# Kernel optimization log

Measured on AMD Instinct MI355X. Metric: run time of the kernel, lower is better.

The kernel has to match this reference:

```python
import jax, jax.numpy as jnp
import numpy as np

N_NODES = 100000
N_EDGES = 800000
F_IN = 128
H1, C1 = 8, 32
N_CLS = 40
NEG_SLOPE = 0.2


def setup_inputs() -> dict:
    key = jax.random.key(0)
    ks = jax.random.split(key, 10)
    s = 1.0 / np.sqrt(F_IN)
    s2 = 1.0 / np.sqrt(H1 * C1)
    return {
        "x": jax.random.normal(ks[0], (N_NODES, F_IN), jnp.float32),
        "edge_index": jax.random.randint(ks[1], (2, N_EDGES), 0, N_NODES, jnp.int64),
        "W1": jax.random.normal(ks[2], (F_IN, H1 * C1), jnp.float32) * s,
        "a_src1": jax.random.normal(ks[3], (H1, C1), jnp.float32) * s2,
        "a_dst1": jax.random.normal(ks[4], (H1, C1), jnp.float32) * s2,
        "b1": jnp.zeros((H1 * C1,), jnp.float32),
        "W2": jax.random.normal(ks[5], (H1 * C1, N_CLS), jnp.float32) * s2,
        "a_src2": jax.random.normal(ks[6], (1, N_CLS), jnp.float32) * 0.1,
        "a_dst2": jax.random.normal(ks[7], (1, N_CLS), jnp.float32) * 0.1,
        "b2": jnp.zeros((N_CLS,), jnp.float32),
    }


def gat_conv(x, src, dst, W, a_src, a_dst, b, heads, out_ch, concat):
    n = x.shape[0]
    h = (x @ W).reshape(n, heads, out_ch)            # [N,H,C]
    alpha_s = jnp.einsum("nhc,hc->nh", h, a_src)     # [N,H]
    alpha_d = jnp.einsum("nhc,hc->nh", h, a_dst)
    e = alpha_s[src] + alpha_d[dst]                  # [E,H]
    e = jax.nn.leaky_relu(e, NEG_SLOPE)
    # per-destination segment softmax (stable)
    m = jax.ops.segment_max(e, dst, num_segments=n)  # [N,H]
    e = jnp.exp(e - m[dst])
    denom = jax.ops.segment_sum(e, dst, num_segments=n)
    alpha = e / (denom[dst] + 1e-16)                 # [E,H]
    msg = alpha[:, :, None] * h[src]                 # [E,H,C]
    out = jax.ops.segment_sum(msg, dst, num_segments=n)  # [N,H,C]
    out = out.reshape(n, heads * out_ch) if concat else out.mean(axis=1)
    return out + b


def reference(x, edge_index, W1, a_src1, a_dst1, b1, W2, a_src2, a_dst2, b2):
    n = x.shape[0]
    # PyG GATConv default add_self_loops=True
    loop = jnp.arange(n, dtype=edge_index.dtype)
    src = jnp.concatenate([edge_index[0], loop])
    dst = jnp.concatenate([edge_index[1], loop])
    # dropout layers are identity in eval mode
    h = gat_conv(x, src, dst, W1, a_src1, a_dst1, b1, H1, C1, concat=True)
    h = jax.nn.elu(h)
    out = gat_conv(h, src, dst, W2, a_src2, a_dst2, b2, 1, N_CLS, concat=False)
    return jax.nn.log_softmax(out, axis=1)
```

## Files before the change

kernel.cpp:

```cpp
#include <hip/hip_runtime.h>
#include <hip/hip_fp16.h>
#include <math.h>

#define N_NODESc 100000
#define N_EDGESc 800000
#define F_INc    128
#define HC1c     256
#define NCLSc    40
#define NEG_SLOPEc 0.2f
#define CAPc     40

typedef _Float16 half8 __attribute__((ext_vector_type(8)));
typedef __fp16   f16x2 __attribute__((ext_vector_type(2)));
typedef float    f32x4 __attribute__((ext_vector_type(4)));
typedef float    f32x2 __attribute__((ext_vector_type(2)));

__device__ __forceinline__ unsigned pack_ws(float w, int src) {
    union { f16x2 h; unsigned u; } t;
    t.h = __builtin_amdgcn_cvt_pkrtz(w, w);
    return (unsigned)src | ((t.u & 0xFFFFu) << 17);
}
__device__ __forceinline__ float unpack_w(unsigned pe) {
    union { unsigned short s; __fp16 h; } t;
    t.s = (unsigned short)(pe >> 17);
    return (float)t.h;
}


__global__ void k_init(const float* __restrict__ W1, const float* __restrict__ W2,
                       _Float16* __restrict__ W1Tf, _Float16* __restrict__ W2Tf,
                       int* __restrict__ cnt) {
    if (blockIdx.x < 22) {
        int f = blockIdx.x * 256 + threadIdx.x;
        if (f < 4096) {
            int lane16 = f & 15, quad = (f >> 4) & 3, k0 = (f >> 6) & 3, jt = f >> 8;
            int c = lane16 * 16 + jt;
            int kbase = k0 * 32 + quad * 8;
            _Float16* o = W1Tf + (size_t)f * 8;
            #pragma unroll
            for (int j = 0; j < 8; j++) o[j] = (_Float16)W1[(kbase + j) * HC1c + c];
        } else if (f < 4096 + 1536) {
            int g = f - 4096;
            int lane16 = g & 15, quad = (g >> 4) & 3, k0 = (g >> 6) & 7, jt = g >> 9;
            int c = jt * 16 + lane16;
            int kbase = k0 * 32 + quad * 8;
            _Float16* o = W2Tf + (size_t)g * 8;
            #pragma unroll
            for (int j = 0; j < 8; j++)
                o[j] = (c < NCLSc) ? (_Float16)W2[(kbase + j) * NCLSc + c] : (_Float16)0.f;
        }
    } else {
        int i = (blockIdx.x - 22) * 256 + threadIdx.x;
        if (i < N_NODESc / 4) ((int4*)cnt)[i] = (int4){0, 0, 0, 0};
    }
}


__global__ __launch_bounds__(256) void k_gemm1_scatter(
    const float* __restrict__ x, const _Float16* __restrict__ W1Tf,
    const float* __restrict__ a_src1, const float* __restrict__ a_dst1,
    unsigned char* __restrict__ h1f8, float* __restrict__ as1, float* __restrict__ ad1,
    const int* __restrict__ src, const int* __restrict__ dst,
    int* __restrict__ cnt, int* __restrict__ bucket) {
    if ((blockIdx.x & 1) == 0) {
        int i = (blockIdx.x >> 1) * 256 + threadIdx.x;
        if (i < N_EDGESc / 4) {
            int4 s = ((const int4*)src)[i];
            int4 d = ((const int4*)dst)[i];
            int p0 = atomicAdd(&cnt[d.x], 1);
            int p1 = atomicAdd(&cnt[d.y], 1);
            int p2 = atomicAdd(&cnt[d.z], 1);
            int p3 = atomicAdd(&cnt[d.w], 1);
            if (p0 < CAPc) __builtin_nontemporal_store(s.x, &bucket[d.x * CAPc + p0]);
            if (p1 < CAPc) __builtin_nontemporal_store(s.y, &bucket[d.y * CAPc + p1]);
            if (p2 < CAPc) __builtin_nontemporal_store(s.z, &bucket[d.z * CAPc + p2]);
            if (p3 < CAPc) __builtin_nontemporal_store(s.w, &bucket[d.w * CAPc + p3]);
        }
        return;
    }
    int wave = ((blockIdx.x >> 1) * 256 + (int)threadIdx.x) >> 6;
    int n0 = wave * 16;
    if (n0 >= N_NODESc) return;
    int L = threadIdx.x & 63, lane16 = L & 15, quad = L >> 4;
    f32x4 acc[16];
    #pragma unroll
    for (int jt = 0; jt < 16; jt++) acc[jt] = (f32x4){0.f, 0.f, 0.f, 0.f};
    const float* A = x + (size_t)(n0 + lane16) * F_INc + quad * 8;
    const _Float16* Bf = W1Tf + L * 8;
    #pragma unroll
    for (int k0 = 0; k0 < 4; k0++) {
        float4 f0 = *(const float4*)(A + k0 * 32);
        float4 f1 = *(const float4*)(A + k0 * 32 + 4);
        union { half8 v; f16x2 h[4]; } af;
        af.h[0] = __builtin_amdgcn_cvt_pkrtz(f0.x, f0.y);
        af.h[1] = __builtin_amdgcn_cvt_pkrtz(f0.z, f0.w);
        af.h[2] = __builtin_amdgcn_cvt_pkrtz(f1.x, f1.y);
        af.h[3] = __builtin_amdgcn_cvt_pkrtz(f1.z, f1.w);
        #pragma unroll
        for (int jt = 0; jt < 16; jt++) {
            half8 bf = *(const half8*)(Bf + (jt * 4 + k0) * 512);
            acc[jt] = __builtin_amdgcn_mfma_f32_16x16x32_f16(af.v, bf, acc[jt], 0, 0, 0);
        }
    }
    {
        #pragma unroll
        for (int r = 0; r < 4; r++) {
            uint4 st;
            int d;
            d = __builtin_amdgcn_cvt_pk_fp8_f32(acc[0][r], acc[1][r], 0, false);
            d = __builtin_amdgcn_cvt_pk_fp8_f32(acc[2][r], acc[3][r], d, true);
            st.x = (unsigned)d;
            d = __builtin_amdgcn_cvt_pk_fp8_f32(acc[4][r], acc[5][r], 0, false);
            d = __builtin_amdgcn_cvt_pk_fp8_f32(acc[6][r], acc[7][r], d, true);
            st.y = (unsigned)d;
            d = __builtin_amdgcn_cvt_pk_fp8_f32(acc[8][r], acc[9][r], 0, false);
            d = __builtin_amdgcn_cvt_pk_fp8_f32(acc[10][r], acc[11][r], d, true);
            st.z = (unsigned)d;
            d = __builtin_amdgcn_cvt_pk_fp8_f32(acc[12][r], acc[13][r], 0, false);
            d = __builtin_amdgcn_cvt_pk_fp8_f32(acc[14][r], acc[15][r], d, true);
            st.w = (unsigned)d;
            *(uint4*)(h1f8 + (size_t)(n0 + quad * 4 + r) * HC1c + lane16 * 16) = st;
        }
    }
    {
        float asv[16], adv[16];
        const float4* ap = (const float4*)(a_src1 + lane16 * 16);
        const float4* dp = (const float4*)(a_dst1 + lane16 * 16);
        #pragma unroll
        for (int q = 0; q < 4; q++) {
            float4 a4 = ap[q], d4 = dp[q];
            asv[4*q] = a4.x; asv[4*q+1] = a4.y; asv[4*q+2] = a4.z; asv[4*q+3] = a4.w;
            adv[4*q] = d4.x; adv[4*q+1] = d4.y; adv[4*q+2] = d4.z; adv[4*q+3] = d4.w;
        }
        float ps[4] = {0,0,0,0}, pd[4] = {0,0,0,0};
        #pragma unroll
        for (int jt = 0; jt < 16; jt++) {
            #pragma unroll
            for (int r = 0; r < 4; r++) {
                ps[r] += acc[jt][r] * asv[jt];
                pd[r] += acc[jt][r] * adv[jt];
            }
        }
        #pragma unroll
        for (int r = 0; r < 4; r++) {
            ps[r] += __shfl_xor(ps[r], 1);
            pd[r] += __shfl_xor(pd[r], 1);
        }
        if ((lane16 & 1) == 0) {
            int h = lane16 >> 1;
            #pragma unroll
            for (int r = 0; r < 4; r++) {
                int n = n0 + quad * 4 + r;
                as1[n * 8 + h] = ps[r];
                ad1[n * 8 + h] = pd[r];
            }
        }
    }
}


__global__ __launch_bounds__(256) void k_agg1_g2(
    const int* __restrict__ cnt, const int* __restrict__ bucket,
    const float* __restrict__ as1, const float* __restrict__ ad1,
    const unsigned char* __restrict__ h1f8, const float* __restrict__ b1,
    const _Float16* __restrict__ W2Tf, const float* __restrict__ a_src2,
    const float* __restrict__ a_dst2, float* __restrict__ h2x,
    float* __restrict__ ad2) {
    __shared__ _Float16 sact[16 * HC1c];
    __shared__ float sp[3][16], sd[3][16];
    int L = threadIdx.x & 63;
    int wid = threadIdx.x >> 6;
    int eL = L >> 3, hL = L & 7;
    int hA = L >> 3;
    float4 bb = ((const float4*)b1)[L];
    #pragma unroll 1
    for (int nn = 0; nn < 4; nn++) {
        int row = wid * 4 + nn;
        int n = blockIdx.x * 16 + row;
        int beg = n * CAPc;
        int end = beg + min(cnt[n], CAPc);
        float ad = ad1[n * 8 + hL];
        float vs = as1[n * 8 + hL] + ad;
        float s_self = (vs > 0.f) ? vs : NEG_SLOPEc * vs;
        float w_self = __expf(s_self);
        unsigned ldself = *((const unsigned*)(h1f8 + (size_t)n * HC1c) + L);
        float ws_c = __shfl(w_self, hA);
        f32x2 wsv = (f32x2){ws_c, ws_c};
        f32x2 accA = wsv * __builtin_amdgcn_cvt_pk_f32_fp8((int)ldself, false);
        f32x2 accB = wsv * __builtin_amdgcn_cvt_pk_f32_fp8((int)ldself, true);
        float d_lane = 0.f;
        for (int base = beg; base < end; base += 16) {
            int m = min(16, end - base);
            int src0 = 0, src1 = 0;
            float w0 = 0.f, w1 = 0.f;
            if (eL < m) {
                src0 = bucket[base + eL];
                float v = as1[src0 * 8 + hL] + ad;
                float s0 = (v > 0.f) ? v : NEG_SLOPEc * v;
                w0 = __expf(s0);
            }
            if (eL + 8 < m) {
                src1 = bucket[base + eL + 8];
                float v = as1[src1 * 8 + hL] + ad;
                float s1 = (v > 0.f) ? v : NEG_SLOPEc * v;
                w1 = __expf(s1);
            }
            d_lane += w0 + w1;
            unsigned pk0 = pack_ws(w0, src0);
            unsigned pk1 = pack_ws(w1, src1);
            #pragma unroll
            for (int r = 0; r < 4; r++) {
                int e0 = r * 4;
                if (e0 < m) {
                    unsigned pk = (e0 < 8) ? pk0 : pk1;
                    unsigned pe[4]; unsigned ld[4];
                    #pragma unroll
                    for (int j = 0; j < 4; j++)
                        pe[j] = __shfl(pk, ((e0 + j) & 7) * 8 + hA);
                    #pragma unroll
                    for (int j = 0; j < 4; j++)
                        ld[j] = *((const unsigned*)(h1f8 + (size_t)(pe[j] & 0x1FFFFu) * HC1c) + L);
                    #pragma unroll
                    for (int j = 0; j < 4; j++) {
                        float w = unpack_w(pe[j]);
                        f32x2 wv = (f32x2){w, w};
                        f32x2 lo = __builtin_amdgcn_cvt_pk_f32_fp8((int)ld[j], false);
                        f32x2 hi = __builtin_amdgcn_cvt_pk_f32_fp8((int)ld[j], true);
                        asm("v_pk_fma_f32 %0, %1, %2, %0" : "+v"(accA) : "v"(wv), "v"(lo));
                        asm("v_pk_fma_f32 %0, %1, %2, %0" : "+v"(accB) : "v"(wv), "v"(hi));
                    }
                }
            }
        }
        d_lane += __shfl_xor(d_lane, 8);
        d_lane += __shfl_xor(d_lane, 16);
        d_lane += __shfl_xor(d_lane, 32);
        float d_run = d_lane + w_self;
        float inv = __builtin_amdgcn_rcpf(d_run + 1e-16f);
        float inv_h = __shfl(inv, hA);
        float o0 = accA[0] * inv_h + bb.x;
        float o1 = accA[1] * inv_h + bb.y;
        float o2 = accB[0] * inv_h + bb.z;
        float o3 = accB[1] * inv_h + bb.w;
        o0 = (o0 > 0.f) ? o0 : (__expf(o0) - 1.f);
        o1 = (o1 > 0.f) ? o1 : (__expf(o1) - 1.f);
        o2 = (o2 > 0.f) ? o2 : (__expf(o2) - 1.f);
        o3 = (o3 > 0.f) ? o3 : (__expf(o3) - 1.f);
        union { uint2 u; f16x2 h[2]; } st;
        st.h[0] = __builtin_amdgcn_cvt_pkrtz(o0, o1);
        st.h[1] = __builtin_amdgcn_cvt_pkrtz(o2, o3);
        unsigned bofs = ((unsigned)(row * 512 + L * 8)) ^ ((unsigned)(row & 7) << 4);
        *(uint2*)((char*)sact + bofs) = st.u;
    }
    __syncthreads();
    if (wid < 3) {
        int jt = wid;
        int lane16 = L & 15, quad = L >> 4;
        int n0 = blockIdx.x * 16;
        f32x4 acc = (f32x4){0.f, 0.f, 0.f, 0.f};
        const _Float16* Bf = W2Tf + L * 8;
        unsigned rmask = ((unsigned)(lane16 & 7) << 4);
        #pragma unroll
        for (int k0 = 0; k0 < 8; k0++) {
            unsigned abofs = ((unsigned)(lane16 * 512 + quad * 16 + k0 * 64)) ^ rmask;
            half8 af = *(const half8*)((const char*)sact + abofs);
            half8 bf = *(const half8*)(Bf + (jt * 8 + k0) * 512);
            acc = __builtin_amdgcn_mfma_f32_16x16x32_f16(af, bf, acc, 0, 0, 0);
        }
        int col = jt * 16 + lane16;
        float ws = (col < NCLSc) ? a_src2[col] : 0.f;
        float wd = (col < NCLSc) ? a_dst2[col] : 0.f;
        float ps[4], pd[4];
        #pragma unroll
        for (int r = 0; r < 4; r++) {
            float v = acc[r];
            int n = n0 + quad * 4 + r;
            if (col < NCLSc)
                ((_Float16*)(h2x + (size_t)n * 32))[2 + col] = (_Float16)v;
            ps[r] = v * ws; pd[r] = v * wd;
        }
        #pragma unroll
        for (int r = 0; r < 4; r++) {
            float s = ps[r], d = pd[r];
            s += __shfl_xor(s, 1); d += __shfl_xor(d, 1);
            s += __shfl_xor(s, 2); d += __shfl_xor(d, 2);
            s += __shfl_xor(s, 4); d += __shfl_xor(d, 4);
            s += __shfl_xor(s, 8); d += __shfl_xor(d, 8);
            if (lane16 == 0) {
                sp[jt][quad * 4 + r] = s;
                sd[jt][quad * 4 + r] = d;
            }
        }
    }
    __syncthreads();
    if (threadIdx.x < 16) {
        int r = threadIdx.x;
        int n = blockIdx.x * 16 + r;
        h2x[(size_t)n * 32] = sp[0][r] + sp[1][r] + sp[2][r];
        ad2[n] = sd[0][r] + sd[1][r] + sd[2][r];
    }
}


__global__ __launch_bounds__(256) void k_agg2(
    const int* __restrict__ cnt, const int* __restrict__ bucket,
    const float* __restrict__ h2x, const float* __restrict__ ad2,
    const float* __restrict__ b2, float* __restrict__ out) {
    int L = threadIdx.x & 63;
    int half = L >> 5, l32 = L & 31;
    int n = blockIdx.x * 8 + (int)(threadIdx.x >> 6) * 2 + half;
    int beg = n * CAPc;
    int end = beg + min(cnt[n], CAPc);
    float ad = ad2[n];
    float vs = h2x[(size_t)n * 32] + ad;
    float s_self = (vs > 0.f) ? vs : NEG_SLOPEc * vs;
    float w_self = __expf(s_self);
    f16x2 acc2 = (f16x2){(__fp16)0.f, (__fp16)0.f};
    if (l32 < 20) {
        union { unsigned u; f16x2 h; } pk0;
        pk0.u = ((const unsigned*)(h2x + (size_t)n * 32))[1 + l32];
        f16x2 wsv = __builtin_amdgcn_cvt_pkrtz(w_self, w_self);
        acc2 = wsv * pk0.h;
    }
    float d_lane = 0.f;
    for (int base = beg; base < end; base += 32) {
        int m = min(32, end - base);
        int src = 0; float w = 0.f;
        if (l32 < m) {
            src = bucket[base + l32];
            float v = h2x[(size_t)src * 32] + ad;
            float s = (v > 0.f) ? v : NEG_SLOPEc * v;
            w = __expf(s);
        }
        d_lane += w;
        unsigned pk = pack_ws(w, src);
        for (int jb = 0; jb < m; jb += 12) {
            unsigned pe[12];
            #pragma unroll
            for (int j = 0; j < 12; j++) {
                int e = jb + j;
                unsigned t = __shfl(pk, half * 32 + (e & 31));
                pe[j] = (e < m) ? t : 0u;
            }
            unsigned ldv[12];
            #pragma unroll
            for (int j = 0; j < 12; j++)
                ldv[j] = (l32 < 20)
                    ? ((const unsigned*)(h2x + (size_t)(pe[j] & 0x1FFFFu) * 32))[1 + l32]
                    : 0u;
            #pragma unroll
            for (int j = 0; j < 12; j++) {
                float w_j = unpack_w(pe[j]);
                f16x2 we2 = __builtin_amdgcn_cvt_pkrtz(w_j, w_j);
                union { unsigned u; f16x2 h; } pkv; pkv.u = ldv[j];
                acc2 += we2 * pkv.h;
            }
        }
    }
    #pragma unroll
    for (int o = 16; o; o >>= 1) d_lane += __shfl_xor(d_lane, o);
    float d_run = d_lane + w_self;
    float vx = -INFINITY, vy = -INFINITY;
    if (l32 < 20) {
        float2 bb = ((const float2*)b2)[l32];
        float inv = __builtin_amdgcn_rcpf(d_run + 1e-16f);
        vx = (float)acc2[0] * inv + bb.x;
        vy = (float)acc2[1] * inv + bb.y;
    }
    float mv = fmaxf(vx, vy);
    #pragma unroll
    for (int o = 16; o; o >>= 1) mv = fmaxf(mv, __shfl_xor(mv, o));
    float ex = (l32 < 20) ? __expf(vx - mv) + __expf(vy - mv) : 0.f;
    #pragma unroll
    for (int o = 16; o; o >>= 1) ex += __shfl_xor(ex, o);
    float ls = __logf(ex);
    if (l32 < 20) {
        float2 o2; o2.x = vx - mv - ls; o2.y = vy - mv - ls;
        ((float2*)(out + (size_t)n * NCLSc))[l32] = o2;
    }
}


extern "C" void kernel_launch(void* const* d_in, const int* in_sizes, int n_in,
                              void* d_out, int out_size, void* d_ws, size_t ws_size,
                              hipStream_t stream) {
    const float* x    = (const float*)d_in[0];
    const int*   ei   = (const int*)d_in[1];
    const float* W1   = (const float*)d_in[2];
    const float* as1w = (const float*)d_in[3];
    const float* ad1w = (const float*)d_in[4];
    const float* b1   = (const float*)d_in[5];
    const float* W2   = (const float*)d_in[6];
    const float* as2w = (const float*)d_in[7];
    const float* ad2w = (const float*)d_in[8];
    const float* b2   = (const float*)d_in[9];
    float* out = (float*)d_out;

    char* p = (char*)d_ws;
    unsigned char* h1f8 = (unsigned char*)p; p += (size_t)N_NODESc * HC1c;
    _Float16* W1Tf  = (_Float16*)p; p += (size_t)4096 * 8 * 2;
    _Float16* W2Tf  = (_Float16*)p; p += (size_t)1536 * 8 * 2;
    float* a_s1 = (float*)p; p += (size_t)N_NODESc * 8 * 4;
    float* a_d1 = (float*)p; p += (size_t)N_NODESc * 8 * 4;
    float* h2x  = (float*)p; p += (size_t)N_NODESc * 32 * 4;
    float* a_d2 = (float*)p; p += (size_t)N_NODESc * 4;
    int* cnt    = (int*)p;   p += (size_t)N_NODESc * 4;
    int* bucket = (int*)p;   p += (size_t)N_NODESc * CAPc * 4;
    (void)ws_size; (void)in_sizes; (void)n_in; (void)out_size;

    const int* src = ei;
    const int* dst = ei + N_EDGESc;

    k_init<<<22 + (N_NODESc / 4 + 255) / 256, 256, 0, stream>>>(W1, W2, W1Tf, W2Tf, cnt);

    int nwave_blk = ((N_NODESc + 15) / 16 + 3) / 4;
    k_gemm1_scatter<<<nwave_blk * 2, 256, 0, stream>>>(
        x, W1Tf, as1w, ad1w, h1f8, a_s1, a_d1, src, dst, cnt, bucket);

    k_agg1_g2<<<N_NODESc / 16, 256, 0, stream>>>(
        cnt, bucket, a_s1, a_d1, h1f8, b1, W2Tf, as2w, ad2w, h2x, a_d2);

    k_agg2<<<N_NODESc / 8, 256, 0, stream>>>(cnt, bucket, h2x, a_d2, b2, out);
}
```

Measured before the change: 258.9 us.

## Software-pipeline neighbor index and score loads across nodes in layer-1 aggregation

The layer-1 aggregation loop now prefetches the next node's degree, first 16 neighbor indices, source attention scores and self/dest scores while the current node is processed. All 16 gathers of the first chunk are issued together before any FMAs run, so more loads are in flight at once, and the remaining chunks fall back to the old loop. The aim is to hide the dependent bucket→as1→h1 gather latency chain. The cost is higher register pressure from the 16-entry pe/ld arrays and the prefetched state, which may lower occupancy.

```diff
diff --git a/kernel.cpp b/kernel.cpp
--- a/kernel.cpp
+++ b/kernel.cpp
@@ -173,59 +173,125 @@
     int eL = L >> 3, hL = L & 7;
     int hA = L >> 3;
     float4 bb = ((const float4*)b1)[L];
+    int nbase = blockIdx.x * 16 + wid * 4;
+
+    int4 cn = *(const int4*)&cnt[nbase];
+    int deg_c = min(cn.x, CAPc);
+    int src0_c = 0, src1_c = 0;
+    if (eL < deg_c) src0_c = bucket[nbase * CAPc + eL];
+    if (eL + 8 < deg_c) src1_c = bucket[nbase * CAPc + eL + 8];
+    float sv0_c = (eL < deg_c) ? as1[src0_c * 8 + hL] : 0.f;
+    float sv1_c = (eL + 8 < deg_c) ? as1[src1_c * 8 + hL] : 0.f;
+    float selfa_c = as1[nbase * 8 + hL];
+    float ad_c = ad1[nbase * 8 + hL];
+
     #pragma unroll 1
     for (int nn = 0; nn < 4; nn++) {
-        int row = wid * 4 + nn;
-        int n = blockIdx.x * 16 + row;
-        int beg = n * CAPc;
-        int end = beg + min(cnt[n], CAPc);
-        float ad = ad1[n * 8 + hL];
-        float vs = as1[n * 8 + hL] + ad;
-        float s_self = (vs > 0.f) ? vs : NEG_SLOPEc * vs;
+        int n = nbase + nn;
+        int deg = deg_c;
+        int src0 = src0_c, src1 = src1_c;
+        float sv0 = sv0_c, sv1 = sv1_c;
+        float selfa = selfa_c, ad = ad_c;
+        int m1 = min(16, deg);
+        float w0 = 0.f, w1 = 0.f;
+        if (eL < m1) {
+            float v = sv0 + ad;
+            float s = (v > 0.f) ? v : NEG_SLOPEc * v;
+            w0 = __expf(s);
+        }
+        if (eL + 8 < m1) {
+            float v = sv1 + ad;
+            float s = (v > 0.f) ? v : NEG_SLOPEc * v;
+            w1 = __expf(s);
+        }
+        float d_lane = w0 + w1;
+        float vsf = selfa + ad;
+        float s_self = (vsf > 0.f) ? vsf : NEG_SLOPEc * vsf;
         float w_self = __expf(s_self);
+        unsigned pk0 = pack_ws(w0, src0);
+        unsigned pk1 = pack_ws(w1, src1);
+        unsigned pe[16];
+        #pragma unroll
+        for (int j = 0; j < 16; j++)
+            pe[j] = __shfl((j < 8) ? pk0 : pk1, (j & 7) * 8 + hA);
+        unsigned ld[16];
+        #pragma unroll
+        for (int r = 0; r < 4; r++) {
+            if (r * 4 < m1) {
+                #pragma unroll
+                for (int j = 0; j < 4; j++)
+                    ld[r*4+j] = *((const unsigned*)(h1f8 + (size_t)(pe[r*4+j] & 0x1FFFFu) * HC1c) + L);
+            }
+        }
         unsigned ldself = *((const unsigned*)(h1f8 + (size_t)n * HC1c) + L);
+        if (nn < 3) {
+            int degn = (nn == 0) ? cn.y : (nn == 1) ? cn.z : cn.w;
+            deg_c = min(degn, CAPc);
+            int begn = (n + 1) * CAPc;
+            src0_c = 0; src1_c = 0;
+            if (eL < deg_c) src0_c = bucket[begn + eL];
+            if (eL + 8 < deg_c) src1_c = bucket[begn + eL + 8];
+            sv0_c = (eL < deg_c) ? as1[src0_c * 8 + hL] : 0.f;
+            sv1_c = (eL + 8 < deg_c) ? as1[src1_c * 8 + hL] : 0.f;
+            selfa_c = as1[(n + 1) * 8 + hL];
+            ad_c = ad1[(n + 1) * 8 + hL];
+        }
         float ws_c = __shfl(w_self, hA);
         f32x2 wsv = (f32x2){ws_c, ws_c};
         f32x2 accA = wsv * __builtin_amdgcn_cvt_pk_f32_fp8((int)ldself, false);
         f32x2 accB = wsv * __builtin_amdgcn_cvt_pk_f32_fp8((int)ldself, true);
-        float d_lane = 0.f;
-        for (int base = beg; base < end; base += 16) {
-            int m = min(16, end - base);
-            int src0 = 0, src1 = 0;
-            float w0 = 0.f, w1 = 0.f;
+        #pragma unroll
+        for (int r = 0; r < 4; r++) {
+            if (r * 4 < m1) {
+                #pragma unroll
+                for (int j = 0; j < 4; j++) {
+                    float w = unpack_w(pe[r*4+j]);
+                    f32x2 wv = (f32x2){w, w};
+                    f32x2 lo = __builtin_amdgcn_cvt_pk_f32_fp8((int)ld[r*4+j], false);
+                    f32x2 hi = __builtin_amdgcn_cvt_pk_f32_fp8((int)ld[r*4+j], true);
+                    asm("v_pk_fma_f32 %0, %1, %2, %0" : "+v"(accA) : "v"(wv), "v"(lo));
+                    asm("v_pk_fma_f32 %0, %1, %2, %0" : "+v"(accB) : "v"(wv), "v"(hi));
+                }
+            }
+        }
+        int beg = n * CAPc;
+        for (int base = beg + 16; base < beg + deg; base += 16) {
+            int m = min(16, beg + deg - base);
+            int ts0 = 0, ts1 = 0;
+            float tw0 = 0.f, tw1 = 0.f;
             if (eL < m) {
-                src0 = bucket[base + eL];
-                float v = as1[src0 * 8 + hL] + ad;
-                float s0 = (v > 0.f) ? v : NEG_SLOPEc * v;
-                w0 = __expf(s0);
+                ts0 = bucket[base + eL];
+                float v = as1[ts0 * 8 + hL] + ad;
+                float s = (v > 0.f) ? v : NEG_SLOPEc * v;
+                tw0 = __expf(s);
             }
             if (eL + 8 < m) {
-                src1 = bucket[base + eL + 8];
-                float v = as1[src1 * 8 + hL] + ad;
-                float s1 = (v > 0.f) ? v : NEG_SLOPEc * v;
-                w1 = __expf(s1);
-            }
-            d_lane += w0 + w1;
-            unsigned pk0 = pack_ws(w0, src0);
-            unsigned pk1 = pack_ws(w1, src1);
+                ts1 = bucket[base + eL + 8];
+                float v = as1[ts1 * 8 + hL] + ad;
+                float s = (v > 0.f) ? v : NEG_SLOPEc * v;
+                tw1 = __expf(s);
+            }
+            d_lane += tw0 + tw1;
+            unsigned tpk0 = pack_ws(tw0, ts0);
+            unsigned tpk1 = pack_ws(tw1, ts1);
             #pragma unroll
             for (int r = 0; r < 4; r++) {
                 int e0 = r * 4;
                 if (e0 < m) {
-                    unsigned pk = (e0 < 8) ? pk0 : pk1;
-                    unsigned pe[4]; unsigned ld[4];
+                    unsigned pk = (e0 < 8) ? tpk0 : tpk1;
+                    unsigned tpe[4]; unsigned tld[4];
                     #pragma unroll
                     for (int j = 0; j < 4; j++)
-                        pe[j] = __shfl(pk, ((e0 + j) & 7) * 8 + hA);
+                        tpe[j] = __shfl(pk, ((e0 + j) & 7) * 8 + hA);
                     #pragma unroll
                     for (int j = 0; j < 4; j++)
-                        ld[j] = *((const unsigned*)(h1f8 + (size_t)(pe[j] & 0x1FFFFu) * HC1c) + L);
+                        tld[j] = *((const unsigned*)(h1f8 + (size_t)(tpe[j] & 0x1FFFFu) * HC1c) + L);
                     #pragma unroll
                     for (int j = 0; j < 4; j++) {
-                        float w = unpack_w(pe[j]);
+                        float w = unpack_w(tpe[j]);
                         f32x2 wv = (f32x2){w, w};
-                        f32x2 lo = __builtin_amdgcn_cvt_pk_f32_fp8((int)ld[j], false);
-                        f32x2 hi = __builtin_amdgcn_cvt_pk_f32_fp8((int)ld[j], true);
+                        f32x2 lo = __builtin_amdgcn_cvt_pk_f32_fp8((int)tld[j], false);
+                        f32x2 hi = __builtin_amdgcn_cvt_pk_f32_fp8((int)tld[j], true);
                         asm("v_pk_fma_f32 %0, %1, %2, %0" : "+v"(accA) : "v"(wv), "v"(lo));
                         asm("v_pk_fma_f32 %0, %1, %2, %0" : "+v"(accB) : "v"(wv), "v"(hi));
                     }
@@ -249,6 +315,7 @@
         union { uint2 u; f16x2 h[2]; } st;
         st.h[0] = __builtin_amdgcn_cvt_pkrtz(o0, o1);
         st.h[1] = __builtin_amdgcn_cvt_pkrtz(o2, o3);
+        int row = wid * 4 + nn;
         unsigned bofs = ((unsigned)(row * 512 + L * 8)) ^ ((unsigned)(row & 7) << 4);
         *(uint2*)((char*)sact + bofs) = st.u;
     }
```

Result: slower. 265.4 us (+2.5%).
